# Optimization experiments

Measured on AMD Instinct MI355X. Metric: run time of the kernel, lower is better.

The kernel has to match this reference:

```python
import jax, jax.numpy as jnp
import numpy as np

# dims
B, T = 2, 256            # batch, seq_len
V, H_CP, R = 512, 2, 2   # vocab, CP horizon, CP rank
E, L, NH, NPOS = 768, 12, 12, 1024  # n_embd, n_layer, n_head, max positions
HD = E // NH             # head dim = 64


def _ln(x, g, b, eps=1e-5):
    m = jnp.mean(x, -1, keepdims=True)
    v = jnp.mean((x - m) ** 2, -1, keepdims=True)
    return (x - m) * jax.lax.rsqrt(v + eps) * g + b


def setup_inputs() -> dict:
    key = jax.random.key(0)
    ks = jax.random.split(key, 10)
    s = 0.02  # GPT2 init std
    n = lambda k, sh: s * jax.random.normal(k, sh, jnp.float32)
    return {
        "input_ids": jax.random.randint(ks[0], (B, T), 0, V, dtype=jnp.int32),
        "wte": n(ks[1], (V, E)),
        "wpe": n(ks[2], (NPOS, E)),
        "ln1_g": jnp.ones((L, E), jnp.float32), "ln1_b": jnp.zeros((L, E), jnp.float32),
        "ln2_g": jnp.ones((L, E), jnp.float32), "ln2_b": jnp.zeros((L, E), jnp.float32),
        "w_qkv": n(ks[3], (L, E, 3 * E)), "b_qkv": jnp.zeros((L, 3 * E), jnp.float32),
        "w_ao": n(ks[4], (L, E, E)), "b_ao": jnp.zeros((L, E), jnp.float32),
        "w_fc": n(ks[5], (L, E, 4 * E)), "b_fc": jnp.zeros((L, 4 * E), jnp.float32),
        "w_mo": n(ks[6], (L, 4 * E, E)), "b_mo": jnp.zeros((L, E), jnp.float32),
        "lnf_g": jnp.ones((E,), jnp.float32), "lnf_b": jnp.zeros((E,), jnp.float32),
        "w_cp": n(ks[7], (E, H_CP * V * R)), "b_cp": jnp.zeros((H_CP * V * R,), jnp.float32),
    }


def reference(input_ids, wte, wpe, ln1_g, ln1_b, ln2_g, ln2_b, w_qkv, b_qkv,
              w_ao, b_ao, w_fc, b_fc, w_mo, b_mo, lnf_g, lnf_b, w_cp, b_cp):
    # --- GPT2 transformer body (eval mode: dropout inactive) ---
    h = wte[input_ids] + wpe[:T]                      # (B,T,E)
    causal = jnp.tril(jnp.ones((T, T), bool))
    inv_sqrt_hd = float(1.0 / np.sqrt(HD))

    def block(h, p):
        l1g, l1b, l2g, l2b, wq, bq, wa, ba, wf, bf, wm, bm = p
        x = _ln(h, l1g, l1b)
        qkv = x @ wq + bq                             # (B,T,3E)
        q, k, v = jnp.split(qkv, 3, axis=-1)
        q = q.reshape(B, T, NH, HD).transpose(0, 2, 1, 3)
        k = k.reshape(B, T, NH, HD).transpose(0, 2, 1, 3)
        v = v.reshape(B, T, NH, HD).transpose(0, 2, 1, 3)
        att = jnp.einsum('bhqd,bhkd->bhqk', q, k) * inv_sqrt_hd
        att = jnp.where(causal, att, jnp.float32(-1e9))
        att = jax.nn.softmax(att, axis=-1)
        o = jnp.einsum('bhqk,bhkd->bhqd', att, v).transpose(0, 2, 1, 3).reshape(B, T, E)
        h = h + o @ wa + ba
        x = _ln(h, l2g, l2b)
        h = h + jax.nn.gelu(x @ wf + bf, approximate=True) @ wm + bm  # gelu_new
        return h, None

    h, _ = jax.lax.scan(block, h, (ln1_g, ln1_b, ln2_g, ln2_b, w_qkv, b_qkv,
                                   w_ao, b_ao, w_fc, b_fc, w_mo, b_mo))
    h = _ln(h, lnf_g, lnf_b)                          # last_hidden_state

    # --- CP joint distribution: sum_r outer(f0_r, f1_r), then positivity(exp) ---
    cp = (h.reshape(B * T, E) @ w_cp + b_cp).reshape(B * T, H_CP, V, R)
    scores = jnp.einsum('nir,njr->nij', cp[:, 0], cp[:, 1])  # (B*T, V, V)
    mjd = jnp.exp(scores).reshape(B, T, V, V)[:, :-H_CP].reshape(-1, V, V)

    # --- windowed targets: targets[b,t,h] = input_ids[b, t+1+h] ---
    off = jnp.arange(T - H_CP)[:, None] + 1 + jnp.arange(H_CP)[None, :]
    tgt = input_ids[:, off].reshape(-1, H_CP)         # (B*(T-H), H)

    # --- entropy loss over unnormalized joint: mean(log Z - log p_target) ---
    n = mjd.shape[0]
    p_t = mjd[jnp.arange(n), tgt[:, 0], tgt[:, 1]]
    Z = mjd.sum((1, 2))
    loss = jnp.mean(jnp.log(Z) - jnp.log(p_t))
    return loss
```

## Files before the change

kernel.cpp:

```cpp
#include <hip/hip_runtime.h>

typedef unsigned short u16;
typedef short short8 __attribute__((ext_vector_type(8)));
typedef float f32x4 __attribute__((ext_vector_type(4)));

constexpr int B_  = 2;
constexpr int T_  = 256;
constexpr int V_  = 512;
constexpr int E_  = 768;
constexpr int L_  = 12;
constexpr int NH_ = 12;
constexpr int HD_ = 64;
constexpr int E3_ = 3 * E_;
constexpr int E4_ = 4 * E_;
constexpr int CPD_ = 2048;
constexpr int NTOK_ = B_ * T_;
constexpr int NVALID_ = B_ * (T_ - 2);

__device__ __forceinline__ u16 f2b(float f) {
    union { float f; unsigned int u; } c; c.f = f;
    unsigned int r = (c.u + 0x7FFFu + ((c.u >> 16) & 1u)) >> 16; return (u16)r;
}

__global__ __launch_bounds__(256) void embed_k(const int* __restrict__ ids,
    const float* __restrict__ wte, const float* __restrict__ wpe,
    float* __restrict__ h) {
    int n = blockIdx.x;
    int t = n % T_;
    int tok = ids[n];
    for (int e = threadIdx.x; e < E_; e += 256)
        h[n * E_ + e] = wte[tok * E_ + e] + wpe[t * E_ + e];
}

__global__ __launch_bounds__(256) void ln_k(const float* __restrict__ in,
    const float* __restrict__ g, const float* __restrict__ bta,
    u16* __restrict__ out) {
    int n = blockIdx.x;
    int tid = threadIdx.x;
    const float* x = in + (size_t)n * E_;
    float v0 = x[tid], v1 = x[tid + 256], v2 = x[tid + 512];
    __shared__ float red[256];
    red[tid] = v0 + v1 + v2;
    __syncthreads();
    for (int o = 128; o > 0; o >>= 1) { if (tid < o) red[tid] += red[tid + o]; __syncthreads(); }
    float mean = red[0] * (1.0f / E_);
    __syncthreads();
    float d0 = v0 - mean, d1 = v1 - mean, d2 = v2 - mean;
    red[tid] = d0 * d0 + d1 * d1 + d2 * d2;
    __syncthreads();
    for (int o = 128; o > 0; o >>= 1) { if (tid < o) red[tid] += red[tid + o]; __syncthreads(); }
    float rstd = rsqrtf(red[0] * (1.0f / E_) + 1e-5f);
    u16* y = out + (size_t)n * E_;
    y[tid]       = f2b(d0 * rstd * g[tid]       + bta[tid]);
    y[tid + 256] = f2b(d1 * rstd * g[tid + 256] + bta[tid + 256]);
    y[tid + 512] = f2b(d2 * rstd * g[tid + 512] + bta[tid + 512]);
}

__global__ __launch_bounds__(512) void mgemm_k(const u16* __restrict__ A,
    const float* __restrict__ W, const float* __restrict__ bias,
    float* __restrict__ outF, u16* __restrict__ outB,
    int K, int KC, int N, int mode) {
    __shared__ u16 As[128 * 40];
    __shared__ u16 Bs[64 * 40];
    int tid = threadIdx.x, lane = tid & 63, wid = tid >> 6;
    int ln15 = lane & 15, quad = lane >> 4;
    int col0 = blockIdx.x * 64, row0 = blockIdx.y * 128;
    int kz = blockIdx.z, kbase = kz * KC;
    int ar = tid >> 2, ak = (tid & 3) * 8;
    const u16* Ag = A + (size_t)(row0 + ar) * K + kbase + ak;
    u16* Aw = &As[ar * 40 + ak];
    int wk4 = (tid >> 6) * 4;
    const float* Wg = W + (size_t)(kbase + wk4) * N + col0 + lane;
    u16* Bw = &Bs[lane * 40 + wk4];
    int wr = (wid >> 1) * 32, wc = (wid & 1) * 32;

    f32x4 zero = {0.f, 0.f, 0.f, 0.f};
    f32x4 acc[2][2];
    acc[0][0] = zero; acc[0][1] = zero; acc[1][0] = zero; acc[1][1] = zero;

    for (int k0 = 0; k0 < KC; k0 += 32) {
        uint4 av = *(const uint4*)(Ag + k0);
        float w0 = Wg[(size_t)(k0 + 0) * N];
        float w1 = Wg[(size_t)(k0 + 1) * N];
        float w2 = Wg[(size_t)(k0 + 2) * N];
        float w3 = Wg[(size_t)(k0 + 3) * N];
        unsigned int r0, r1;
        asm("v_cvt_pk_bf16_f32 %0, %1, %2" : "=v"(r0) : "v"(w0), "v"(w1));
        asm("v_cvt_pk_bf16_f32 %0, %1, %2" : "=v"(r1) : "v"(w2), "v"(w3));
        __syncthreads();
        *(uint4*)Aw = av;
        uint2 bw; bw.x = r0; bw.y = r1;
        *(uint2*)Bw = bw;
        __syncthreads();
        short8 af[2], bf[2];
#pragma unroll
        for (int mt = 0; mt < 2; mt++)
            af[mt] = *(const short8*)&As[(wr + mt * 16 + ln15) * 40 + quad * 8];
#pragma unroll
        for (int nt = 0; nt < 2; nt++)
            bf[nt] = *(const short8*)&Bs[(wc + nt * 16 + ln15) * 40 + quad * 8];
#pragma unroll
        for (int mt = 0; mt < 2; mt++)
#pragma unroll
            for (int nt = 0; nt < 2; nt++)
                acc[mt][nt] = __builtin_amdgcn_mfma_f32_16x16x32_bf16(
                    af[mt], bf[nt], acc[mt][nt], 0, 0, 0);
    }
#pragma unroll
    for (int mt = 0; mt < 2; mt++) {
#pragma unroll
        for (int nt = 0; nt < 2; nt++) {
            int c = col0 + wc + nt * 16 + ln15;
            if (mode == 0) {
                float bb = (kz == 0) ? bias[c] : 0.f;
#pragma unroll
                for (int r = 0; r < 4; r++) {
                    int rw = row0 + wr + mt * 16 + quad * 4 + r;
                    atomicAdd(&outF[(size_t)rw * N + c], acc[mt][nt][r] + bb);
                }
            } else {
                float bb = bias[c];
#pragma unroll
                for (int r = 0; r < 4; r++) {
                    int rw = row0 + wr + mt * 16 + quad * 4 + r;
                    float u = acc[mt][nt][r] + bb;
                    float inner = 0.7978845608028654f * (u + 0.044715f * u * u * u);
                    float v = 0.5f * u * (1.0f + tanhf(inner));
                    outB[(size_t)rw * N + c] = f2b(v);
                }
            }
        }
    }
}

constexpr int KSTR_ = 72;
constexpr int PSTR_ = 264;
__global__ __launch_bounds__(256) void fattn_k(const float* __restrict__ qkv,
    u16* __restrict__ o) {
    __shared__ u16 Ks[256 * KSTR_];
    __shared__ u16 Vt[64 * PSTR_];
    __shared__ u16 Ps[64 * PSTR_];
    int qt = blockIdx.x;
    int bh = blockIdx.y;
    int hh = bh % NH_, b = bh / NH_;
    int tid = threadIdx.x, lane = tid & 63, wid = tid >> 6;
    int ln15 = lane & 15, quad = lane >> 4;

    int sr = tid >> 4, sd = (tid & 15) * 4;
    const float* Kg = qkv + (size_t)(b * T_) * E3_ + E_ + hh * HD_;
    const float* Vg = qkv + (size_t)(b * T_) * E3_ + 2 * E_ + hh * HD_;
#pragma unroll
    for (int pass = 0; pass < 16; pass++) {
        int rr = sr + pass * 16;
        float4 kv = *(const float4*)&Kg[(size_t)rr * E3_ + sd];
        unsigned int c0, c1;
        asm("v_cvt_pk_bf16_f32 %0, %1, %2" : "=v"(c0) : "v"(kv.x), "v"(kv.y));
        asm("v_cvt_pk_bf16_f32 %0, %1, %2" : "=v"(c1) : "v"(kv.z), "v"(kv.w));
        uint2 pk; pk.x = c0; pk.y = c1;
        *(uint2*)&Ks[rr * KSTR_ + sd] = pk;
        float4 vv = *(const float4*)&Vg[(size_t)rr * E3_ + sd];
        Vt[(sd + 0) * PSTR_ + rr] = f2b(vv.x);
        Vt[(sd + 1) * PSTR_ + rr] = f2b(vv.y);
        Vt[(sd + 2) * PSTR_ + rr] = f2b(vv.z);
        Vt[(sd + 3) * PSTR_ + rr] = f2b(vv.w);
    }

    const float* Qg = qkv + (size_t)(b * T_ + qt * 64 + wid * 16 + ln15) * E3_ + hh * HD_;
    short8 qf[2];
#pragma unroll
    for (int ks = 0; ks < 2; ks++) {
        const float* qp = Qg + ks * 32 + quad * 8;
        union { short8 s8; unsigned int u[4]; } uq;
#pragma unroll
        for (int i = 0; i < 4; i++) {
            float a0 = qp[2 * i], a1 = qp[2 * i + 1];
            asm("v_cvt_pk_bf16_f32 %0, %1, %2" : "=v"(uq.u[i]) : "v"(a0), "v"(a1));
        }
        qf[ks] = uq.s8;
    }

    __syncthreads();

    f32x4 s[16];
#pragma unroll
    for (int nt = 0; nt < 16; nt++) s[nt] = (f32x4){0.f, 0.f, 0.f, 0.f};
#pragma unroll
    for (int ks = 0; ks < 2; ks++) {
#pragma unroll
        for (int nt = 0; nt < 16; nt++) {
            short8 kf = *(const short8*)&Ks[(nt * 16 + ln15) * KSTR_ + ks * 32 + quad * 8];
            s[nt] = __builtin_amdgcn_mfma_f32_16x16x32_bf16(qf[ks], kf, s[nt], 0, 0, 0);
        }
    }

#pragma unroll
    for (int r = 0; r < 4; r++) {
        int q = qt * 64 + wid * 16 + quad * 4 + r;
        float m = -1e30f;
#pragma unroll
        for (int nt = 0; nt < 16; nt++) {
            int j = nt * 16 + ln15;
            float sv = (j <= q) ? s[nt][r] * 0.125f : -1e9f;
            s[nt][r] = sv;
            m = fmaxf(m, sv);
        }
        m = fmaxf(m, __shfl_xor(m, 1));
        m = fmaxf(m, __shfl_xor(m, 2));
        m = fmaxf(m, __shfl_xor(m, 4));
        m = fmaxf(m, __shfl_xor(m, 8));
        float sum = 0.f;
#pragma unroll
        for (int nt = 0; nt < 16; nt++) {
            float p = __expf(s[nt][r] - m);
            s[nt][r] = p;
            sum += p;
        }
        sum += __shfl_xor(sum, 1);
        sum += __shfl_xor(sum, 2);
        sum += __shfl_xor(sum, 4);
        sum += __shfl_xor(sum, 8);
        float inv = 1.0f / sum;
#pragma unroll
        for (int nt = 0; nt < 16; nt++) s[nt][r] *= inv;
    }

#pragma unroll
    for (int nt = 0; nt < 16; nt++)
#pragma unroll
        for (int r = 0; r < 4; r++)
            Ps[(wid * 16 + quad * 4 + r) * PSTR_ + nt * 16 + ln15] = f2b(s[nt][r]);

    __syncthreads();

    f32x4 oacc[4];
#pragma unroll
    for (int dt = 0; dt < 4; dt++) oacc[dt] = (f32x4){0.f, 0.f, 0.f, 0.f};
#pragma unroll
    for (int ks = 0; ks < 8; ks++) {
        short8 pf = *(const short8*)&Ps[(wid * 16 + ln15) * PSTR_ + ks * 32 + quad * 8];
#pragma unroll
        for (int dt = 0; dt < 4; dt++) {
            short8 vf = *(const short8*)&Vt[(dt * 16 + ln15) * PSTR_ + ks * 32 + quad * 8];
            oacc[dt] = __builtin_amdgcn_mfma_f32_16x16x32_bf16(pf, vf, oacc[dt], 0, 0, 0);
        }
    }

#pragma unroll
    for (int dt = 0; dt < 4; dt++) {
#pragma unroll
        for (int r = 0; r < 4; r++) {
            int q = qt * 64 + wid * 16 + quad * 4 + r;
            o[(size_t)(b * T_ + q) * E_ + hh * HD_ + dt * 16 + ln15] = f2b(oacc[dt][r]);
        }
    }
}

__global__ __launch_bounds__(256) void zloss_k(const float* __restrict__ cp,
    const int* __restrict__ ids, float* __restrict__ lossv) {
    int n = blockIdx.x;
    int b = n / (T_ - 2), t = n % (T_ - 2);
    int nf = b * T_ + t;
    const float* a = cp + (size_t)nf * CPD_;
    const float* bb = a + 1024;
    __shared__ float A0[V_], A1[V_], B0[V_], B1[V_];
    __shared__ float red[256];
    int tid = threadIdx.x;
    for (int v = tid; v < V_; v += 256) {
        A0[v] = a[2 * v]; A1[v] = a[2 * v + 1];
        B0[v] = bb[2 * v]; B1[v] = bb[2 * v + 1];
    }
    __syncthreads();
    float acc = 0.f;
    for (int j = tid; j < V_; j += 256) {
        float b0 = B0[j], b1 = B1[j];
        for (int i = 0; i < V_; i++)
            acc += __expf(A0[i] * b0 + A1[i] * b1);
    }
    red[tid] = acc; __syncthreads();
    for (int off = 128; off > 0; off >>= 1) { if (tid < off) red[tid] += red[tid + off]; __syncthreads(); }
    if (tid == 0) {
        int t0 = ids[b * T_ + t + 1];
        int t1 = ids[b * T_ + t + 2];
        float score = A0[t0] * B0[t1] + A1[t0] * B1[t1];
        lossv[n] = logf(red[0]) - score;
    }
}

__global__ __launch_bounds__(256) void reduce_k(const float* __restrict__ lossv,
    unsigned int* __restrict__ out) {
    __shared__ float red[256];
    int tid = threadIdx.x;
    float s = 0.f;
    for (int i = tid; i < NVALID_; i += 256) s += lossv[i];
    red[tid] = s; __syncthreads();
    for (int off = 128; off > 0; off >>= 1) { if (tid < off) red[tid] += red[tid + off]; __syncthreads(); }
    if (tid == 0) {
        float loss = red[0] / (float)NVALID_;
        union { float f; unsigned int u; } cv; cv.f = loss;
        unsigned int b = (cv.u + 0x7FFFu + ((cv.u >> 16) & 1u)) >> 16;
        out[0] = (b << 16) | b;
    }
}

extern "C" void kernel_launch(void* const* d_in, const int* in_sizes, int n_in,
                              void* d_out, int out_size, void* d_ws, size_t ws_size,
                              hipStream_t stream) {
    const int*   ids  = (const int*)d_in[0];
    const float* wte  = (const float*)d_in[1];
    const float* wpe  = (const float*)d_in[2];
    const float* ln1g = (const float*)d_in[3];
    const float* ln1b = (const float*)d_in[4];
    const float* ln2g = (const float*)d_in[5];
    const float* ln2b = (const float*)d_in[6];
    const float* wqkv = (const float*)d_in[7];
    const float* bqkv = (const float*)d_in[8];
    const float* wao  = (const float*)d_in[9];
    const float* bao  = (const float*)d_in[10];
    const float* wfc  = (const float*)d_in[11];
    const float* bfc  = (const float*)d_in[12];
    const float* wmo  = (const float*)d_in[13];
    const float* bmo  = (const float*)d_in[14];
    const float* lnfg = (const float*)d_in[15];
    const float* lnfb = (const float*)d_in[16];
    const float* wcp  = (const float*)d_in[17];
    const float* bcp  = (const float*)d_in[18];

    char* p = (char*)d_ws;
    float* h    = (float*)p; p += (size_t)NTOK_ * E_ * 4;
    u16*   x    = (u16*)p;   p += (size_t)NTOK_ * E_ * 2;
    u16*   aob  = (u16*)p;   p += (size_t)NTOK_ * E_ * 2;
    u16*   fcb  = (u16*)p;   p += (size_t)NTOK_ * E4_ * 2;
    float* bigF = (float*)p; p += (size_t)NTOK_ * E3_ * 4;
    float* lossv = (float*)p; p += 4096;
    float* qkvF = bigF;
    float* cpF  = bigF;

    embed_k<<<NTOK_, 256, 0, stream>>>(ids, wte, wpe, h);
    for (int l = 0; l < L_; l++) {
        ln_k<<<NTOK_, 256, 0, stream>>>(h, ln1g + l * E_, ln1b + l * E_, x);
        hipMemsetAsync(qkvF, 0, (size_t)NTOK_ * E3_ * 4, stream);
        mgemm_k<<<dim3(E3_ / 64, 4, 2), 512, 0, stream>>>(
            x, wqkv + (size_t)l * E_ * E3_, bqkv + l * E3_, qkvF, nullptr, E_, 384, E3_, 0);
        fattn_k<<<dim3(4, B_ * NH_), 256, 0, stream>>>(qkvF, aob);
        mgemm_k<<<dim3(E_ / 64, 4, 6), 512, 0, stream>>>(
            aob, wao + (size_t)l * E_ * E_, bao + l * E_, h, nullptr, E_, 128, E_, 0);
        ln_k<<<NTOK_, 256, 0, stream>>>(h, ln2g + l * E_, ln2b + l * E_, x);
        mgemm_k<<<dim3(E4_ / 64, 4, 1), 512, 0, stream>>>(
            x, wfc + (size_t)l * E_ * E4_, bfc + l * E4_, nullptr, fcb, E_, 768, E4_, 1);
        mgemm_k<<<dim3(E_ / 64, 4, 8), 512, 0, stream>>>(
            fcb, wmo + (size_t)l * E4_ * E_, bmo + l * E_, h, nullptr, E4_, 384, E_, 0);
    }
    ln_k<<<NTOK_, 256, 0, stream>>>(h, lnfg, lnfb, x);
    hipMemsetAsync(cpF, 0, (size_t)NTOK_ * CPD_ * 4, stream);
    mgemm_k<<<dim3(CPD_ / 64, 4, 2), 512, 0, stream>>>(
        x, wcp, bcp, cpF, nullptr, E_, 384, CPD_, 0);
    zloss_k<<<NVALID_, 256, 0, stream>>>(cpF, ids, lossv);
    reduce_k<<<1, 256, 0, stream>>>(lossv, (unsigned int*)d_out);
}
```

Baseline: 1.441 ms.

## Replace atomic split-K with partial buffers fused into residual LayerNorm

The GEMM epilogues that used atomicAdd into zero-filled buffers now write split-K partials to separate buffers. The next LayerNorm kernel adds both partials into the residual stream, which removes the memsets and atomics. The QKV GEMM now writes bf16 directly, so attention no longer converts fp32 at load time. GEMM tiles shrink to 64x64 with 256 threads, each thread loading 8 weight rows per step, and the split-K factors change. This trades atomic traffic for extra partial-buffer reads and more, smaller blocks.

After: 1.700 ms. 17.9% more time.

```diff
diff --git a/kernel.cpp b/kernel.cpp
--- a/kernel.cpp
+++ b/kernel.cpp
@@ -16,6 +16,7 @@
 constexpr int CPD_ = 2048;
 constexpr int NTOK_ = B_ * T_;
 constexpr int NVALID_ = B_ * (T_ - 2);
+constexpr size_t PN_ = (size_t)NTOK_ * E_;
 
 __device__ __forceinline__ u16 f2b(float f) {
     union { float f; unsigned int u; } c; c.f = f;
@@ -32,13 +33,22 @@
         h[n * E_ + e] = wte[tok * E_ + e] + wpe[t * E_ + e];
 }
 
-__global__ __launch_bounds__(256) void ln_k(const float* __restrict__ in,
+__global__ __launch_bounds__(256) void ln_res_k(float* __restrict__ h,
+    const float* __restrict__ p0, const float* __restrict__ p1,
     const float* __restrict__ g, const float* __restrict__ bta,
     u16* __restrict__ out) {
     int n = blockIdx.x;
     int tid = threadIdx.x;
-    const float* x = in + (size_t)n * E_;
-    float v0 = x[tid], v1 = x[tid + 256], v2 = x[tid + 512];
+    size_t off = (size_t)n * E_;
+    float v0, v1, v2;
+    if (p0) {
+        v0 = h[off + tid]       + p0[off + tid]       + p1[off + tid];
+        v1 = h[off + tid + 256] + p0[off + tid + 256] + p1[off + tid + 256];
+        v2 = h[off + tid + 512] + p0[off + tid + 512] + p1[off + tid + 512];
+        h[off + tid] = v0; h[off + tid + 256] = v1; h[off + tid + 512] = v2;
+    } else {
+        v0 = h[off + tid]; v1 = h[off + tid + 256]; v2 = h[off + tid + 512];
+    }
     __shared__ float red[256];
     red[tid] = v0 + v1 + v2;
     __syncthreads();
@@ -50,28 +60,28 @@
     __syncthreads();
     for (int o = 128; o > 0; o >>= 1) { if (tid < o) red[tid] += red[tid + o]; __syncthreads(); }
     float rstd = rsqrtf(red[0] * (1.0f / E_) + 1e-5f);
-    u16* y = out + (size_t)n * E_;
+    u16* y = out + off;
     y[tid]       = f2b(d0 * rstd * g[tid]       + bta[tid]);
     y[tid + 256] = f2b(d1 * rstd * g[tid + 256] + bta[tid + 256]);
     y[tid + 512] = f2b(d2 * rstd * g[tid + 512] + bta[tid + 512]);
 }
 
-__global__ __launch_bounds__(512) void mgemm_k(const u16* __restrict__ A,
+__global__ __launch_bounds__(256) void mgemm_k(const u16* __restrict__ A,
     const float* __restrict__ W, const float* __restrict__ bias,
     float* __restrict__ outF, u16* __restrict__ outB,
     int K, int KC, int N, int mode) {
-    __shared__ u16 As[128 * 40];
+    __shared__ u16 As[64 * 40];
     __shared__ u16 Bs[64 * 40];
     int tid = threadIdx.x, lane = tid & 63, wid = tid >> 6;
     int ln15 = lane & 15, quad = lane >> 4;
-    int col0 = blockIdx.x * 64, row0 = blockIdx.y * 128;
+    int col0 = blockIdx.x * 64, row0 = blockIdx.y * 64;
     int kz = blockIdx.z, kbase = kz * KC;
     int ar = tid >> 2, ak = (tid & 3) * 8;
     const u16* Ag = A + (size_t)(row0 + ar) * K + kbase + ak;
     u16* Aw = &As[ar * 40 + ak];
-    int wk4 = (tid >> 6) * 4;
-    const float* Wg = W + (size_t)(kbase + wk4) * N + col0 + lane;
-    u16* Bw = &Bs[lane * 40 + wk4];
+    int kg = (tid >> 6) * 8;
+    const float* Wg = W + (size_t)(kbase + kg) * N + col0 + lane;
+    u16* Bw = &Bs[lane * 40 + kg];
     int wr = (wid >> 1) * 32, wc = (wid & 1) * 32;
 
     f32x4 zero = {0.f, 0.f, 0.f, 0.f};
@@ -80,17 +90,17 @@
 
     for (int k0 = 0; k0 < KC; k0 += 32) {
         uint4 av = *(const uint4*)(Ag + k0);
-        float w0 = Wg[(size_t)(k0 + 0) * N];
-        float w1 = Wg[(size_t)(k0 + 1) * N];
-        float w2 = Wg[(size_t)(k0 + 2) * N];
-        float w3 = Wg[(size_t)(k0 + 3) * N];
-        unsigned int r0, r1;
-        asm("v_cvt_pk_bf16_f32 %0, %1, %2" : "=v"(r0) : "v"(w0), "v"(w1));
-        asm("v_cvt_pk_bf16_f32 %0, %1, %2" : "=v"(r1) : "v"(w2), "v"(w3));
+        float w[8];
+#pragma unroll
+        for (int i = 0; i < 8; i++) w[i] = Wg[(size_t)(k0 + i) * N];
+        uint4 bv;
+        asm("v_cvt_pk_bf16_f32 %0, %1, %2" : "=v"(bv.x) : "v"(w[0]), "v"(w[1]));
+        asm("v_cvt_pk_bf16_f32 %0, %1, %2" : "=v"(bv.y) : "v"(w[2]), "v"(w[3]));
+        asm("v_cvt_pk_bf16_f32 %0, %1, %2" : "=v"(bv.z) : "v"(w[4]), "v"(w[5]));
+        asm("v_cvt_pk_bf16_f32 %0, %1, %2" : "=v"(bv.w) : "v"(w[6]), "v"(w[7]));
         __syncthreads();
         *(uint4*)Aw = av;
-        uint2 bw; bw.x = r0; bw.y = r1;
-        *(uint2*)Bw = bw;
+        *(uint4*)Bw = bv;
         __syncthreads();
         short8 af[2], bf[2];
 #pragma unroll
@@ -112,13 +122,13 @@
         for (int nt = 0; nt < 2; nt++) {
             int c = col0 + wc + nt * 16 + ln15;
             if (mode == 0) {
-                float bb = (kz == 0) ? bias[c] : 0.f;
+                float bb = bias[c];
 #pragma unroll
                 for (int r = 0; r < 4; r++) {
                     int rw = row0 + wr + mt * 16 + quad * 4 + r;
-                    atomicAdd(&outF[(size_t)rw * N + c], acc[mt][nt][r] + bb);
+                    outF[(size_t)rw * N + c] = acc[mt][nt][r] + bb;
                 }
-            } else {
+            } else if (mode == 1) {
                 float bb = bias[c];
 #pragma unroll
                 for (int r = 0; r < 4; r++) {
@@ -128,6 +138,21 @@
                     float v = 0.5f * u * (1.0f + tanhf(inner));
                     outB[(size_t)rw * N + c] = f2b(v);
                 }
+            } else if (mode == 2) {
+                float bb = (kz == 0) ? bias[c] : 0.f;
+                float* dst = outF + (size_t)kz * NTOK_ * N;
+#pragma unroll
+                for (int r = 0; r < 4; r++) {
+                    int rw = row0 + wr + mt * 16 + quad * 4 + r;
+                    dst[(size_t)rw * N + c] = acc[mt][nt][r] + bb;
+                }
+            } else {
+                float bb = bias[c];
+#pragma unroll
+                for (int r = 0; r < 4; r++) {
+                    int rw = row0 + wr + mt * 16 + quad * 4 + r;
+                    outB[(size_t)rw * N + c] = f2b(acc[mt][nt][r] + bb);
+                }
             }
         }
     }
@@ -135,7 +160,7 @@
 
 constexpr int KSTR_ = 72;
 constexpr int PSTR_ = 264;
-__global__ __launch_bounds__(256) void fattn_k(const float* __restrict__ qkv,
+__global__ __launch_bounds__(256) void fattn_k(const u16* __restrict__ qkv,
     u16* __restrict__ o) {
     __shared__ u16 Ks[256 * KSTR_];
     __shared__ u16 Vt[64 * PSTR_];
@@ -147,37 +172,25 @@
     int ln15 = lane & 15, quad = lane >> 4;
 
     int sr = tid >> 4, sd = (tid & 15) * 4;
-    const float* Kg = qkv + (size_t)(b * T_) * E3_ + E_ + hh * HD_;
-    const float* Vg = qkv + (size_t)(b * T_) * E3_ + 2 * E_ + hh * HD_;
+    const u16* Kg = qkv + (size_t)(b * T_) * E3_ + E_ + hh * HD_;
+    const u16* Vg = qkv + (size_t)(b * T_) * E3_ + 2 * E_ + hh * HD_;
 #pragma unroll
     for (int pass = 0; pass < 16; pass++) {
         int rr = sr + pass * 16;
-        float4 kv = *(const float4*)&Kg[(size_t)rr * E3_ + sd];
-        unsigned int c0, c1;
-        asm("v_cvt_pk_bf16_f32 %0, %1, %2" : "=v"(c0) : "v"(kv.x), "v"(kv.y));
-        asm("v_cvt_pk_bf16_f32 %0, %1, %2" : "=v"(c1) : "v"(kv.z), "v"(kv.w));
-        uint2 pk; pk.x = c0; pk.y = c1;
-        *(uint2*)&Ks[rr * KSTR_ + sd] = pk;
-        float4 vv = *(const float4*)&Vg[(size_t)rr * E3_ + sd];
-        Vt[(sd + 0) * PSTR_ + rr] = f2b(vv.x);
-        Vt[(sd + 1) * PSTR_ + rr] = f2b(vv.y);
-        Vt[(sd + 2) * PSTR_ + rr] = f2b(vv.z);
-        Vt[(sd + 3) * PSTR_ + rr] = f2b(vv.w);
-    }
-
-    const float* Qg = qkv + (size_t)(b * T_ + qt * 64 + wid * 16 + ln15) * E3_ + hh * HD_;
+        uint2 kv = *(const uint2*)&Kg[(size_t)rr * E3_ + sd];
+        *(uint2*)&Ks[rr * KSTR_ + sd] = kv;
+        ushort4 vv = *(const ushort4*)&Vg[(size_t)rr * E3_ + sd];
+        Vt[(sd + 0) * PSTR_ + rr] = vv.x;
+        Vt[(sd + 1) * PSTR_ + rr] = vv.y;
+        Vt[(sd + 2) * PSTR_ + rr] = vv.z;
+        Vt[(sd + 3) * PSTR_ + rr] = vv.w;
+    }
+
+    const u16* Qg = qkv + (size_t)(b * T_ + qt * 64 + wid * 16 + ln15) * E3_ + hh * HD_;
     short8 qf[2];
 #pragma unroll
-    for (int ks = 0; ks < 2; ks++) {
-        const float* qp = Qg + ks * 32 + quad * 8;
-        union { short8 s8; unsigned int u[4]; } uq;
-#pragma unroll
-        for (int i = 0; i < 4; i++) {
-            float a0 = qp[2 * i], a1 = qp[2 * i + 1];
-            asm("v_cvt_pk_bf16_f32 %0, %1, %2" : "=v"(uq.u[i]) : "v"(a0), "v"(a1));
-        }
-        qf[ks] = uq.s8;
-    }
+    for (int ks = 0; ks < 2; ks++)
+        qf[ks] = *(const short8*)&Qg[ks * 32 + quad * 8];
 
     __syncthreads();
 
@@ -330,30 +343,30 @@
     u16*   x    = (u16*)p;   p += (size_t)NTOK_ * E_ * 2;
     u16*   aob  = (u16*)p;   p += (size_t)NTOK_ * E_ * 2;
     u16*   fcb  = (u16*)p;   p += (size_t)NTOK_ * E4_ * 2;
-    float* bigF = (float*)p; p += (size_t)NTOK_ * E3_ * 4;
+    u16*   qkvB = (u16*)p;   p += (size_t)NTOK_ * E3_ * 2;
+    float* pbuf = (float*)p; p += 2 * PN_ * 4;
+    float* cpF  = (float*)p; p += (size_t)NTOK_ * CPD_ * 4;
     float* lossv = (float*)p; p += 4096;
-    float* qkvF = bigF;
-    float* cpF  = bigF;
 
     embed_k<<<NTOK_, 256, 0, stream>>>(ids, wte, wpe, h);
     for (int l = 0; l < L_; l++) {
-        ln_k<<<NTOK_, 256, 0, stream>>>(h, ln1g + l * E_, ln1b + l * E_, x);
-        hipMemsetAsync(qkvF, 0, (size_t)NTOK_ * E3_ * 4, stream);
-        mgemm_k<<<dim3(E3_ / 64, 4, 2), 512, 0, stream>>>(
-            x, wqkv + (size_t)l * E_ * E3_, bqkv + l * E3_, qkvF, nullptr, E_, 384, E3_, 0);
-        fattn_k<<<dim3(4, B_ * NH_), 256, 0, stream>>>(qkvF, aob);
-        mgemm_k<<<dim3(E_ / 64, 4, 6), 512, 0, stream>>>(
-            aob, wao + (size_t)l * E_ * E_, bao + l * E_, h, nullptr, E_, 128, E_, 0);
-        ln_k<<<NTOK_, 256, 0, stream>>>(h, ln2g + l * E_, ln2b + l * E_, x);
-        mgemm_k<<<dim3(E4_ / 64, 4, 1), 512, 0, stream>>>(
-            x, wfc + (size_t)l * E_ * E4_, bfc + l * E4_, nullptr, fcb, E_, 768, E4_, 1);
-        mgemm_k<<<dim3(E_ / 64, 4, 8), 512, 0, stream>>>(
-            fcb, wmo + (size_t)l * E4_ * E_, bmo + l * E_, h, nullptr, E4_, 384, E_, 0);
-    }
-    ln_k<<<NTOK_, 256, 0, stream>>>(h, lnfg, lnfb, x);
-    hipMemsetAsync(cpF, 0, (size_t)NTOK_ * CPD_ * 4, stream);
-    mgemm_k<<<dim3(CPD_ / 64, 4, 2), 512, 0, stream>>>(
-        x, wcp, bcp, cpF, nullptr, E_, 384, CPD_, 0);
+        ln_res_k<<<NTOK_, 256, 0, stream>>>(h, l ? pbuf : nullptr, l ? pbuf + PN_ : nullptr,
+                                            ln1g + l * E_, ln1b + l * E_, x);
+        mgemm_k<<<dim3(E3_ / 64, 8, 1), 256, 0, stream>>>(
+            x, wqkv + (size_t)l * E_ * E3_, bqkv + l * E3_, nullptr, qkvB, E_, E_, E3_, 3);
+        fattn_k<<<dim3(4, B_ * NH_), 256, 0, stream>>>(qkvB, aob);
+        mgemm_k<<<dim3(E_ / 64, 8, 2), 256, 0, stream>>>(
+            aob, wao + (size_t)l * E_ * E_, bao + l * E_, pbuf, nullptr, E_, 384, E_, 2);
+        ln_res_k<<<NTOK_, 256, 0, stream>>>(h, pbuf, pbuf + PN_,
+                                            ln2g + l * E_, ln2b + l * E_, x);
+        mgemm_k<<<dim3(E4_ / 64, 8, 1), 256, 0, stream>>>(
+            x, wfc + (size_t)l * E_ * E4_, bfc + l * E4_, nullptr, fcb, E_, E_, E4_, 1);
+        mgemm_k<<<dim3(E_ / 64, 8, 2), 256, 0, stream>>>(
+            fcb, wmo + (size_t)l * E4_ * E_, bmo + l * E_, pbuf, nullptr, E4_, 1536, E_, 2);
+    }
+    ln_res_k<<<NTOK_, 256, 0, stream>>>(h, pbuf, pbuf + PN_, lnfg, lnfb, x);
+    mgemm_k<<<dim3(CPD_ / 64, 8, 1), 256, 0, stream>>>(
+        x, wcp, bcp, cpF, nullptr, E_, E_, CPD_, 0);
     zloss_k<<<NVALID_, 256, 0, stream>>>(cpF, ids, lossv);
     reduce_k<<<1, 256, 0, stream>>>(lossv, (unsigned int*)d_out);
 }
```
